# Kernel tuning notes

Hardware: AMD Instinct MI355X
Metric: run time of the kernel (lower is better)

The kernel has to match this reference:

```python
import jax, jax.numpy as jnp
import numpy as np

B, S, D_MODEL, H = 4, 4096, 1024, 16
HD = D_MODEL // H  # 64
KS = 3             # depthwise conv kernel size
EPS = 1e-6


def dw_causal_conv(x, w, b):
    """Causal depthwise conv over seq. x: [B,S,H,Dk], w: [Dk,KS], b: [Dk].
    Matches Conv1d(groups=d_k, padding=KS-1) followed by cropping the last KS-1."""
    s = x.shape[1]
    xp = jnp.pad(x, ((0, 0), (KS - 1, 0), (0, 0), (0, 0)))
    y = b  # broadcast over [B,S,H,Dk]
    for j in range(KS):
        y = y + w[:, j] * xp[:, j:j + s]
    return y


def feature_map(x):
    return jax.nn.elu(x) + 1.0


def setup_inputs() -> dict:
    key = jax.random.key(0)
    ks = jax.random.split(key, 20)
    sc = 0.02
    inp = {
        'query': jax.random.normal(ks[0], (B, S, D_MODEL), jnp.float32),
        'key':   jax.random.normal(ks[1], (B, S, D_MODEL), jnp.float32),
        'value': jax.random.normal(ks[2], (B, S, D_MODEL), jnp.float32),
        'q_w': jax.random.normal(ks[3], (D_MODEL, D_MODEL), jnp.float32) * sc,
        'q_b': jax.random.normal(ks[4], (D_MODEL,), jnp.float32) * sc,
        'k_w': jax.random.normal(ks[5], (D_MODEL, D_MODEL), jnp.float32) * sc,
        'k_b': jax.random.normal(ks[6], (D_MODEL,), jnp.float32) * sc,
        'v_w': jax.random.normal(ks[7], (D_MODEL, D_MODEL), jnp.float32) * sc,
        'v_b': jax.random.normal(ks[8], (D_MODEL,), jnp.float32) * sc,
        'o_w': jax.random.normal(ks[9], (D_MODEL, D_MODEL), jnp.float32) * sc,
        'o_b': jax.random.normal(ks[10], (D_MODEL,), jnp.float32) * sc,
        'qc_w': jax.random.normal(ks[11], (HD, KS), jnp.float32) * 0.3,
        'qc_b': jax.random.normal(ks[12], (HD,), jnp.float32) * 0.02,
        'kc_w': jax.random.normal(ks[13], (HD, KS), jnp.float32) * 0.3,
        'kc_b': jax.random.normal(ks[14], (HD,), jnp.float32) * 0.02,
        'vc_w': jax.random.normal(ks[15], (HD, KS), jnp.float32) * 0.3,
        'vc_b': jax.random.normal(ks[16], (HD,), jnp.float32) * 0.02,
    }
    return inp


def reference(query, key, value, q_w, q_b, k_w, k_b, v_w, v_b, o_w, o_b,
              qc_w, qc_b, kc_w, kc_b, vc_w, vc_b):
    b, s, _ = query.shape
    q = (query @ q_w.T + q_b).reshape(b, s, H, HD)
    k = (key   @ k_w.T + k_b).reshape(b, s, H, HD)
    v = (value @ v_w.T + v_b).reshape(b, s, H, HD)

    q = feature_map(dw_causal_conv(q, qc_w, qc_b))
    k = feature_map(dw_causal_conv(k, kc_w, kc_b))
    v = dw_causal_conv(v, vc_w, vc_b)

    # linear attention: [B,S,H,D] -> [B,H,S,D]
    Q = q.transpose(0, 2, 1, 3)
    K = k.transpose(0, 2, 1, 3)
    V = v.transpose(0, 2, 1, 3)
    KV = jnp.einsum('bhsd,bhse->bhde', K, V)            # [B,H,D,D]
    Z = 1.0 / jnp.einsum('bhsd,bhd->bhs', Q, K.sum(axis=2) + EPS)
    V_new = jnp.einsum('bhde,bhsd,bhs->bhse', KV, Q, Z)  # [B,H,S,D]

    out = V_new.transpose(0, 2, 1, 3).reshape(b, s, D_MODEL)
    return out @ o_w.T + o_b
```

## Files before the change

### kernel.cpp

```cpp
#include <hip/hip_runtime.h>
#include <hip/hip_bf16.h>
#include <math.h>

#define BB 4
#define SS 4096
#define DM 1024
#define HH 16
#define HD 64
#define NTOK (BB * SS)
#define TSZ ((size_t)NTOK * DM)

typedef _Float16 half8 __attribute__((ext_vector_type(8)));
typedef _Float16 half4v __attribute__((ext_vector_type(4)));
typedef float floatx4 __attribute__((ext_vector_type(4)));

__device__ __forceinline__ void gload16(const void* g, void* l) {
  __builtin_amdgcn_global_load_lds(
      (const __attribute__((address_space(1))) void*)g,
      (__attribute__((address_space(3))) void*)l, 16, 0, 0);
}

#define WAIT4 asm volatile("s_waitcnt vmcnt(4)" ::: "memory")
#define WAIT2 asm volatile("s_waitcnt vmcnt(2)" ::: "memory")
#define WAIT0 asm volatile("s_waitcnt vmcnt(0)" ::: "memory")
#define BARR __builtin_amdgcn_s_barrier()

#define MM3(A_, ah_, al_, bh_, bl_)                                   \
  A_ = __builtin_amdgcn_mfma_f32_16x16x32_f16(ah_, bh_, A_, 0, 0, 0); \
  A_ = __builtin_amdgcn_mfma_f32_16x16x32_f16(ah_, bl_, A_, 0, 0, 0); \
  A_ = __builtin_amdgcn_mfma_f32_16x16x32_f16(al_, bh_, A_, 0, 0, 0)

__device__ __forceinline__ void cvhl(const float4 u0, const float4 u1,
                                     half8& h, half8& l) {
  const float a[8] = {u0.x, u0.y, u0.z, u0.w, u1.x, u1.y, u1.z, u1.w};
#pragma unroll
  for (int e = 0; e < 8; ++e) {
    const _Float16 hh = (_Float16)a[e];
    h[e] = hh;
    l[e] = (_Float16)(a[e] - (float)hh);
  }
}

__global__ __launch_bounds__(256) void split_w4(
    const float* __restrict__ w0, const float* __restrict__ w1,
    const float* __restrict__ w2, const float* __restrict__ w3,
    _Float16* __restrict__ hi, _Float16* __restrict__ lo) {
  const int wi = blockIdx.y;
  const float* src = (wi == 0) ? w0 : (wi == 1) ? w1 : (wi == 2) ? w2 : w3;
  const int i = blockIdx.x * 256 + threadIdx.x;
  const size_t off = ((size_t)wi << 20) >> 2;
  const float4 x = ((const float4*)src)[i];
  half4v h, l;
  h.x = (_Float16)x.x; l.x = (_Float16)(x.x - (float)h.x);
  h.y = (_Float16)x.y; l.y = (_Float16)(x.y - (float)h.y);
  h.z = (_Float16)x.z; l.z = (_Float16)(x.z - (float)h.z);
  h.w = (_Float16)x.w; l.w = (_Float16)(x.w - (float)h.w);
  ((half4v*)hi)[off + i] = h;
  ((half4v*)lo)[off + i] = l;
}

__global__ __launch_bounds__(512, 2) void qkv_gemm8(
    const float* __restrict__ Ak, const float* __restrict__ Av,
    const float* __restrict__ Aq, const _Float16* __restrict__ WhiA,
    const _Float16* __restrict__ WloA, const float* __restrict__ bk,
    const float* __restrict__ bv, const float* __restrict__ bq,
    float* __restrict__ Ck, float* __restrict__ Cv, float* __restrict__ Cq) {
  __shared__ float sA[2][256 * 32];
  __shared__ _Float16 sB[2][256 * 64];

  const int z = blockIdx.z;
  const float* A = (z == 0) ? Ak : (z == 1) ? Av : Aq;
  const float* bias = (z == 0) ? bk : (z == 1) ? bv : bq;
  float* C = (z == 0) ? Ck : (z == 1) ? Cv : Cq;
  const _Float16* Whi = WhiA + ((size_t)z << 20);
  const _Float16* Wlo = WloA + ((size_t)z << 20);

  const int t = threadIdx.x;
  const int wav = t >> 6, lane = t & 63;
  const int wr = wav >> 2, wc = wav & 3;

  const int wg = blockIdx.y * 4 + blockIdx.x;
  const int xcd = wg & 7, cidx = wg >> 3;
  const int bm = ((xcd >> 1) * 16 + (cidx >> 1)) * 256;
  const int bn = ((xcd & 1) * 2 + (cidx & 1)) * 256;

  const int lrow = wav * 8 + (lane >> 3);
  const int cpr = (lane & 7) ^ (lane >> 3);
  const float* pA0 = A + (size_t)(bm + lrow) * DM + cpr * 4;
  const _Float16* pB0 =
      ((cpr < 4) ? Whi : Wlo) + (size_t)(bn + lrow) * DM + (cpr & 3) * 8;
  const int ldsArow = wav * 8 * 32;
  const int ldsBrow = wav * 8 * 64;

#define STA(buf, rb, k0) \
  gload16(pA0 + (size_t)(rb) * DM + (k0), &sA[buf][(rb) * 32 + ldsArow])
#define STB(buf, rb, k0) \
  gload16(pB0 + (size_t)(rb) * DM + (k0), &sB[buf][(rb) * 64 + ldsBrow])

  STA(0, 0, 0); STA(0, 64, 0);
  STB(0, 0, 0); STB(0, 64, 0);
  STB(0, 128, 0); STB(0, 192, 0);
  STA(0, 128, 0); STA(0, 192, 0);

  const int fm = lane & 15;
  const int sw = fm & 7;
  const int kq = lane >> 4;
  int baseA[4], baseB[2];
#pragma unroll
  for (int i = 0; i < 4; ++i) baseA[i] = (wr * 64 + i * 16 + fm) * 32;
#pragma unroll
  for (int j = 0; j < 2; ++j) baseB[j] = (wc * 32 + j * 16 + fm) * 64;
  const int aS0 = ((kq * 2) ^ sw) * 4;
  const int aS1 = ((kq * 2 + 1) ^ sw) * 4;
  const int bSh = (kq ^ sw) * 8;
  const int bSl = ((kq + 4) ^ sw) * 8;

  floatx4 acc[2][4][2][2];
#pragma unroll
  for (int qm = 0; qm < 2; ++qm)
#pragma unroll
    for (int i = 0; i < 4; ++i)
#pragma unroll
      for (int qn = 0; qn < 2; ++qn)
#pragma unroll
        for (int j = 0; j < 2; ++j)
          acc[qm][i][qn][j] = (floatx4){0.f, 0.f, 0.f, 0.f};

  half8 ah[4], al[4];

#define READA_Q(cur_, QM)                                       \
  _Pragma("unroll") for (int i_ = 0; i_ < 4; ++i_) {            \
    const float4 u0_ =                                          \
        *(const float4*)&sA[cur_][baseA[i_] + (QM) * 4096 + aS0]; \
    const float4 u1_ =                                          \
        *(const float4*)&sA[cur_][baseA[i_] + (QM) * 4096 + aS1]; \
    cvhl(u0_, u1_, ah[i_], al[i_]);                             \
  }

#define PH_Q(cur_, QM, QN, ...)                                   \
  {                                                               \
    const half8 bh0_ =                                            \
        *(const half8*)&sB[cur_][baseB[0] + (QN) * 8192 + bSh];   \
    const half8 bl0_ =                                            \
        *(const half8*)&sB[cur_][baseB[0] + (QN) * 8192 + bSl];   \
    const half8 bh1_ =                                            \
        *(const half8*)&sB[cur_][baseB[1] + (QN) * 8192 + bSh];   \
    const half8 bl1_ =                                            \
        *(const half8*)&sB[cur_][baseB[1] + (QN) * 8192 + bSl];   \
    __VA_ARGS__;                                                  \
    __builtin_amdgcn_s_setprio(1);                                \
    _Pragma("unroll") for (int i_ = 0; i_ < 4; ++i_) {            \
      MM3(acc[QM][i_][QN][0], ah[i_], al[i_], bh0_, bl0_);        \
      MM3(acc[QM][i_][QN][1], ah[i_], al[i_], bh1_, bl1_);        \
    }                                                             \
    __builtin_amdgcn_s_setprio(0);                                \
  }

  for (int tt = 0; tt < 31; ++tt) {
    const int cur = tt & 1, nxt = cur ^ 1;
    const int k1 = tt * 32 + 32;
    WAIT4; BARR;
    READA_Q(cur, 0);
    PH_Q(cur, 0, 0, STA(nxt, 0, k1); STA(nxt, 64, k1));
    WAIT4; BARR;
    PH_Q(cur, 0, 1, STB(nxt, 0, k1); STB(nxt, 64, k1));
    WAIT4; BARR;
    READA_Q(cur, 1);
    PH_Q(cur, 1, 0, STB(nxt, 128, k1); STB(nxt, 192, k1));
    PH_Q(cur, 1, 1, STA(nxt, 128, k1); STA(nxt, 192, k1));
  }
  WAIT4; BARR;
  READA_Q(1, 0);
  PH_Q(1, 0, 0, (void)0);
  WAIT2; BARR;
  PH_Q(1, 0, 1, (void)0);
  WAIT0; BARR;
  READA_Q(1, 1);
  PH_Q(1, 1, 0, (void)0);
  PH_Q(1, 1, 1, (void)0);

  const int cr = kq * 4;
#pragma unroll
  for (int qm = 0; qm < 2; ++qm)
#pragma unroll
    for (int i = 0; i < 4; ++i) {
      const int grow = bm + qm * 128 + wr * 64 + i * 16 + cr;
#pragma unroll
      for (int qn = 0; qn < 2; ++qn)
#pragma unroll
        for (int j = 0; j < 2; ++j) {
          const int gcol = bn + qn * 128 + wc * 32 + j * 16 + fm;
          const float bo = bias[gcol];
#pragma unroll
          for (int r = 0; r < 4; ++r)
            C[(size_t)(grow + r) * DM + gcol] = acc[qm][i][qn][j][r] + bo;
        }
    }
#undef STA
#undef STB
#undef READA_Q
#undef PH_Q
}

__global__ __launch_bounds__(512, 2) void o_gemm8(
    const _Float16* __restrict__ Ahi, const _Float16* __restrict__ Alo,
    const _Float16* __restrict__ Whi, const _Float16* __restrict__ Wlo,
    const float* __restrict__ bias, float* __restrict__ C) {
  __shared__ _Float16 sA[2][256 * 64];
  __shared__ _Float16 sB[2][256 * 64];

  const int t = threadIdx.x;
  const int wav = t >> 6, lane = t & 63;
  const int wr = wav >> 2, wc = wav & 3;

  const int wg = blockIdx.y * 4 + blockIdx.x;
  const int xcd = wg & 7, cidx = wg >> 3;
  const int bm = ((xcd >> 1) * 16 + (cidx >> 1)) * 256;
  const int bn = ((xcd & 1) * 2 + (cidx & 1)) * 256;

  const int lrow = wav * 8 + (lane >> 3);
  const int cpr = (lane & 7) ^ (lane >> 3);
  const _Float16* pA0 =
      ((cpr < 4) ? Ahi : Alo) + (size_t)(bm + lrow) * DM + (cpr & 3) * 8;
  const _Float16* pB0 =
      ((cpr < 4) ? Whi : Wlo) + (size_t)(bn + lrow) * DM + (cpr & 3) * 8;
  const int ldsRow = wav * 8 * 64;

#define STAO(buf, rb, k0) \
  gload16(pA0 + (size_t)(rb) * DM + (k0), &sA[buf][(rb) * 64 + ldsRow])
#define STBO(buf, rb, k0) \
  gload16(pB0 + (size_t)(rb) * DM + (k0), &sB[buf][(rb) * 64 + ldsRow])

  STAO(0, 0, 0); STAO(0, 64, 0);
  STBO(0, 0, 0); STBO(0, 64, 0);
  STBO(0, 128, 0); STBO(0, 192, 0);
  STAO(0, 128, 0); STAO(0, 192, 0);

  const int fm = lane & 15;
  const int sw = fm & 7;
  const int kq = lane >> 4;
  int baseA[4], baseB[2];
#pragma unroll
  for (int i = 0; i < 4; ++i) baseA[i] = (wr * 64 + i * 16 + fm) * 64;
#pragma unroll
  for (int j = 0; j < 2; ++j) baseB[j] = (wc * 32 + j * 16 + fm) * 64;
  const int bSh = (kq ^ sw) * 8;
  const int bSl = ((kq + 4) ^ sw) * 8;

  floatx4 acc[2][4][2][2];
#pragma unroll
  for (int qm = 0; qm < 2; ++qm)
#pragma unroll
    for (int i = 0; i < 4; ++i)
#pragma unroll
      for (int qn = 0; qn < 2; ++qn)
#pragma unroll
        for (int j = 0; j < 2; ++j)
          acc[qm][i][qn][j] = (floatx4){0.f, 0.f, 0.f, 0.f};

  half8 ah[4], al[4];

#define READA_O(cur_, QM)                                                 \
  _Pragma("unroll") for (int i_ = 0; i_ < 4; ++i_) {                      \
    ah[i_] = *(const half8*)&sA[cur_][baseA[i_] + (QM) * 8192 + bSh];     \
    al[i_] = *(const half8*)&sA[cur_][baseA[i_] + (QM) * 8192 + bSl];     \
  }

#define PH_O(cur_, QM, QN, ...)                                   \
  {                                                               \
    const half8 bh0_ =                                            \
        *(const half8*)&sB[cur_][baseB[0] + (QN) * 8192 + bSh];   \
    const half8 bl0_ =                                            \
        *(const half8*)&sB[cur_][baseB[0] + (QN) * 8192 + bSl];   \
    const half8 bh1_ =                                            \
        *(const half8*)&sB[cur_][baseB[1] + (QN) * 8192 + bSh];   \
    const half8 bl1_ =                                            \
        *(const half8*)&sB[cur_][baseB[1] + (QN) * 8192 + bSl];   \
    __VA_ARGS__;                                                  \
    __builtin_amdgcn_s_setprio(1);                                \
    _Pragma("unroll") for (int i_ = 0; i_ < 4; ++i_) {            \
      MM3(acc[QM][i_][QN][0], ah[i_], al[i_], bh0_, bl0_);        \
      MM3(acc[QM][i_][QN][1], ah[i_], al[i_], bh1_, bl1_);        \
    }                                                             \
    __builtin_amdgcn_s_setprio(0);                                \
  }

  for (int tt = 0; tt < 31; ++tt) {
    const int cur = tt & 1, nxt = cur ^ 1;
    const int k1 = tt * 32 + 32;
    WAIT4; BARR;
    READA_O(cur, 0);
    PH_O(cur, 0, 0, STAO(nxt, 0, k1); STAO(nxt, 64, k1));
    WAIT4; BARR;
    PH_O(cur, 0, 1, STBO(nxt, 0, k1); STBO(nxt, 64, k1));
    WAIT4; BARR;
    READA_O(cur, 1);
    PH_O(cur, 1, 0, STBO(nxt, 128, k1); STBO(nxt, 192, k1));
    PH_O(cur, 1, 1, STAO(nxt, 128, k1); STAO(nxt, 192, k1));
  }
  WAIT4; BARR;
  READA_O(1, 0);
  PH_O(1, 0, 0, (void)0);
  WAIT2; BARR;
  PH_O(1, 0, 1, (void)0);
  WAIT0; BARR;
  READA_O(1, 1);
  PH_O(1, 1, 0, (void)0);
  PH_O(1, 1, 1, (void)0);

  const int cr = kq * 4;
#pragma unroll
  for (int qm = 0; qm < 2; ++qm)
#pragma unroll
    for (int i = 0; i < 4; ++i) {
      const int grow = bm + qm * 128 + wr * 64 + i * 16 + cr;
#pragma unroll
      for (int qn = 0; qn < 2; ++qn)
#pragma unroll
        for (int j = 0; j < 2; ++j) {
          const int gcol = bn + qn * 128 + wc * 32 + j * 16 + fm;
          const float bo = bias[gcol];
#pragma unroll
          for (int r = 0; r < 4; ++r)
            C[(size_t)(grow + r) * DM + gcol] = acc[qm][i][qn][j][r] + bo;
        }
    }
#undef STAO
#undef STBO
#undef READA_O
#undef PH_O
}

__global__ __launch_bounds__(256) void kv_accum_conv(
    const float* __restrict__ Kg, const float* __restrict__ Vg,
    const float* __restrict__ kc_w, const float* __restrict__ kc_b,
    const float* __restrict__ vc_w, const float* __restrict__ vc_b,
    float* __restrict__ KVp, float* __restrict__ Ksp) {
  const int bh = blockIdx.x;
  const int b = bh >> 4, h = bh & 15;
  const int chunk = blockIdx.y;
  const int s0 = chunk * 256;
  const int t = threadIdx.x;
  const int w = t >> 6, lane = t & 63;
  __shared__ float Kr[34][64], Vr[34][64];
  __shared__ float Kc[32][64], Vc[32][64];
  __shared__ float kw0[64], kw1[64], kw2[64], kb_[64];
  __shared__ float vw0[64], vw1[64], vw2[64], vb_[64];

  if (t < 64) {
    kw0[t] = kc_w[t * 3 + 0]; kw1[t] = kc_w[t * 3 + 1]; kw2[t] = kc_w[t * 3 + 2];
    vw0[t] = vc_w[t * 3 + 0]; vw1[t] = vc_w[t * 3 + 1]; vw2[t] = vc_w[t * 3 + 2];
    kb_[t] = kc_b[t]; vb_[t] = vc_b[t];
  }

  const int d0 = w * 16 + (lane >> 4) * 4;
  const int e0 = (lane & 15) * 4;
  float acc[4][4];
#pragma unroll
  for (int i = 0; i < 4; ++i)
#pragma unroll
    for (int j = 0; j < 4; ++j) acc[i][j] = 0.f;
  float4 ks = make_float4(0.f, 0.f, 0.f, 0.f);
  const size_t gbase = (size_t)b * SS * DM + h * HD;

  for (int c = 0; c < 256; c += 32) {
    __syncthreads();
    for (int idx = t; idx < 544; idx += 256) {
      const int row = idx >> 4, col = (idx & 15) * 4;
      const int s = s0 + c - 2 + row;
      float4 k4 = make_float4(0.f, 0.f, 0.f, 0.f);
      float4 v4 = make_float4(0.f, 0.f, 0.f, 0.f);
      if (s >= 0) {
        k4 = *(const float4*)&Kg[gbase + (size_t)s * DM + col];
        v4 = *(const float4*)&Vg[gbase + (size_t)s * DM + col];
      }
      *(float4*)&Kr[row][col] = k4;
      *(float4*)&Vr[row][col] = v4;
    }
    __syncthreads();
    for (int idx = t; idx < 2048; idx += 256) {
      const int row = idx >> 6, dd = idx & 63;
      float yk = kb_[dd] + kw0[dd] * Kr[row][dd] + kw1[dd] * Kr[row + 1][dd] +
                 kw2[dd] * Kr[row + 2][dd];
      Kc[row][dd] = (yk > 0.f) ? (yk + 1.f) : expf(yk);
      Vc[row][dd] = vb_[dd] + vw0[dd] * Vr[row][dd] + vw1[dd] * Vr[row + 1][dd] +
                    vw2[dd] * Vr[row + 2][dd];
    }
    __syncthreads();
#pragma unroll 2
    for (int ss = 0; ss < 32; ++ss) {
      const float4 k4 = *(const float4*)&Kc[ss][d0];
      const float4 v4 = *(const float4*)&Vc[ss][e0];
      ks.x += k4.x; ks.y += k4.y; ks.z += k4.z; ks.w += k4.w;
      const float kk[4] = {k4.x, k4.y, k4.z, k4.w};
      const float vv[4] = {v4.x, v4.y, v4.z, v4.w};
#pragma unroll
      for (int i = 0; i < 4; ++i)
#pragma unroll
        for (int j = 0; j < 4; ++j) acc[i][j] = fmaf(kk[i], vv[j], acc[i][j]);
    }
  }
  float* kvp = &KVp[((size_t)(bh * 16 + chunk)) * 4096];
#pragma unroll
  for (int i = 0; i < 4; ++i) {
    float4 o = make_float4(acc[i][0], acc[i][1], acc[i][2], acc[i][3]);
    *(float4*)&kvp[(d0 + i) * 64 + e0] = o;
  }
  if ((lane & 15) == 0) {
    float* kp = &Ksp[(bh * 16 + chunk) * 64 + d0];
    kp[0] = ks.x; kp[1] = ks.y; kp[2] = ks.z; kp[3] = ks.w;
  }
}

__global__ __launch_bounds__(256) void kv_reduce(
    const float* __restrict__ KVp, const float* __restrict__ Ksp,
    float* __restrict__ KV, float* __restrict__ Ksum) {
  const int bh = blockIdx.x;
  const int t = threadIdx.x;
  for (int i = t; i < 4096; i += 256) {
    float s = 0.f;
#pragma unroll
    for (int c = 0; c < 16; ++c) s += KVp[((size_t)(bh * 16 + c)) * 4096 + i];
    KV[(size_t)bh * 4096 + i] = s;
  }
  if (t < 64) {
    float s = 1e-6f;
#pragma unroll
    for (int c = 0; c < 16; ++c) s += Ksp[(bh * 16 + c) * 64 + t];
    Ksum[bh * 64 + t] = s;
  }
}

__global__ __launch_bounds__(256) void attn_apply_conv(
    const float* __restrict__ Qg, const float* __restrict__ KV,
    const float* __restrict__ Ksum, const float* __restrict__ qc_w,
    const float* __restrict__ qc_b, _Float16* __restrict__ OHi,
    _Float16* __restrict__ OLo) {
  const int bh = blockIdx.x;
  const int b = bh >> 4, h = bh & 15;
  const int s0 = blockIdx.y * 64;
  const int t = threadIdx.x;
  const int w = t >> 6, lane = t & 63;
  __shared__ float Qr[66][64];
  __shared__ float QsT[64][68];
// ... 95 lines not shown
  const float* k_b = (const float*)d_in[6];
  const float* v_w = (const float*)d_in[7];
  const float* v_b = (const float*)d_in[8];
  const float* o_w = (const float*)d_in[9];
  const float* o_b = (const float*)d_in[10];
  const float* qc_w = (const float*)d_in[11];
  const float* qc_b = (const float*)d_in[12];
  const float* kc_w = (const float*)d_in[13];
  const float* kc_b = (const float*)d_in[14];
  const float* vc_w = (const float*)d_in[15];
  const float* vc_b = (const float*)d_in[16];
  float* out = (float*)d_out;

  float* ws = (float*)d_ws;
  float* buf0 = ws;
  float* buf1 = ws + TSZ;
  float* buf2 = ws + 2 * TSZ;
  _Float16* Whi = (_Float16*)(ws + 3 * TSZ);
  _Float16* Wlo = Whi + 4 * (1 << 20);
  float* KVp  = (float*)(Wlo + 4 * (1 << 20));
  float* Ksp  = KVp + (size_t)64 * 16 * 4096;
  float* KV   = Ksp + 64 * 16 * 64;
  float* Ksum = KV + (size_t)64 * 4096;

  _Float16* WhiO = Whi + 3 * (1 << 20);
  _Float16* WloO = Wlo + 3 * (1 << 20);
  _Float16* OHi = (_Float16*)buf0;
  _Float16* OLo = OHi + TSZ;

  const int nW4 = DM * DM / 4;

  split_w4<<<dim3(nW4 / 256, 4), 256, 0, stream>>>(k_w, v_w, q_w, o_w, Whi, Wlo);

  qkv_gemm8<<<dim3(4, 64, 3), 512, 0, stream>>>(
      key, value, query, Whi, Wlo, k_b, v_b, q_b, buf0, buf1, buf2);

  kv_accum_conv<<<dim3(64, 16), 256, 0, stream>>>(buf0, buf1, kc_w, kc_b, vc_w,
                                                  vc_b, KVp, Ksp);
  kv_reduce<<<64, 256, 0, stream>>>(KVp, Ksp, KV, Ksum);

  attn_apply_conv<<<dim3(64, 64), 256, 0, stream>>>(buf2, KV, Ksum, qc_w, qc_b,
                                                    OHi, OLo);

  o_gemm8<<<dim3(4, 64), 512, 0, stream>>>(OHi, OLo, WhiO, WloO, o_b, out);
}
```

Before: 705.5 us.

## Use 32x32 MFMA in GEMMs, merge QKV into one persistent pass, prefetch conv loads

```diff
diff --git a/kernel.cpp b/kernel.cpp
--- a/kernel.cpp
+++ b/kernel.cpp
@@ -13,6 +13,7 @@
 typedef _Float16 half8 __attribute__((ext_vector_type(8)));
 typedef _Float16 half4v __attribute__((ext_vector_type(4)));
 typedef float floatx4 __attribute__((ext_vector_type(4)));
+typedef float floatx16 __attribute__((ext_vector_type(16)));
 
 __device__ __forceinline__ void gload16(const void* g, void* l) {
   __builtin_amdgcn_global_load_lds(
@@ -25,10 +26,10 @@
 #define WAIT0 asm volatile("s_waitcnt vmcnt(0)" ::: "memory")
 #define BARR __builtin_amdgcn_s_barrier()
 
-#define MM3(A_, ah_, al_, bh_, bl_)                                   \
-  A_ = __builtin_amdgcn_mfma_f32_16x16x32_f16(ah_, bh_, A_, 0, 0, 0); \
-  A_ = __builtin_amdgcn_mfma_f32_16x16x32_f16(ah_, bl_, A_, 0, 0, 0); \
-  A_ = __builtin_amdgcn_mfma_f32_16x16x32_f16(al_, bh_, A_, 0, 0, 0)
+#define MM3W(A_, ah_, al_, bh_, bl_)                                   \
+  A_ = __builtin_amdgcn_mfma_f32_32x32x16_f16(ah_, bh_, A_, 0, 0, 0);  \
+  A_ = __builtin_amdgcn_mfma_f32_32x32x16_f16(ah_, bl_, A_, 0, 0, 0);  \
+  A_ = __builtin_amdgcn_mfma_f32_32x32x16_f16(al_, bh_, A_, 0, 0, 0)
 
 __device__ __forceinline__ void cvhl(const float4 u0, const float4 u1,
                                      half8& h, half8& l) {
@@ -59,7 +60,7 @@
   ((half4v*)lo)[off + i] = l;
 }
 
-__global__ __launch_bounds__(512, 2) void qkv_gemm8(
+__global__ __launch_bounds__(512, 2) void qkv_gemm32(
     const float* __restrict__ Ak, const float* __restrict__ Av,
     const float* __restrict__ Aq, const _Float16* __restrict__ WhiA,
     const _Float16* __restrict__ WloA, const float* __restrict__ bk,
@@ -68,13 +69,6 @@
   __shared__ float sA[2][256 * 32];
   __shared__ _Float16 sB[2][256 * 64];
 
-  const int z = blockIdx.z;
-  const float* A = (z == 0) ? Ak : (z == 1) ? Av : Aq;
-  const float* bias = (z == 0) ? bk : (z == 1) ? bv : bq;
-  float* C = (z == 0) ? Ck : (z == 1) ? Cv : Cq;
-  const _Float16* Whi = WhiA + ((size_t)z << 20);
-  const _Float16* Wlo = WloA + ((size_t)z << 20);
-
   const int t = threadIdx.x;
   const int wav = t >> 6, lane = t & 63;
   const int wr = wav >> 2, wc = wav & 3;
@@ -86,123 +80,135 @@
 
   const int lrow = wav * 8 + (lane >> 3);
   const int cpr = (lane & 7) ^ (lane >> 3);
-  const float* pA0 = A + (size_t)(bm + lrow) * DM + cpr * 4;
-  const _Float16* pB0 =
-      ((cpr < 4) ? Whi : Wlo) + (size_t)(bn + lrow) * DM + (cpr & 3) * 8;
+  const float* pA0k = Ak + (size_t)(bm + lrow) * DM + cpr * 4;
+  const float* pA0v = Av + (size_t)(bm + lrow) * DM + cpr * 4;
+  const float* pA0q = Aq + (size_t)(bm + lrow) * DM + cpr * 4;
+  const _Float16* pB0z =
+      ((cpr < 4) ? WhiA : WloA) + (size_t)(bn + lrow) * DM + (cpr & 3) * 8;
   const int ldsArow = wav * 8 * 32;
   const int ldsBrow = wav * 8 * 64;
 
-#define STA(buf, rb, k0) \
-  gload16(pA0 + (size_t)(rb) * DM + (k0), &sA[buf][(rb) * 32 + ldsArow])
-#define STB(buf, rb, k0) \
-  gload16(pB0 + (size_t)(rb) * DM + (k0), &sB[buf][(rb) * 64 + ldsBrow])
-
-  STA(0, 0, 0); STA(0, 64, 0);
-  STB(0, 0, 0); STB(0, 64, 0);
-  STB(0, 128, 0); STB(0, 192, 0);
-  STA(0, 128, 0); STA(0, 192, 0);
-
-  const int fm = lane & 15;
-  const int sw = fm & 7;
-  const int kq = lane >> 4;
-  int baseA[4], baseB[2];
-#pragma unroll
-  for (int i = 0; i < 4; ++i) baseA[i] = (wr * 64 + i * 16 + fm) * 32;
-#pragma unroll
-  for (int j = 0; j < 2; ++j) baseB[j] = (wc * 32 + j * 16 + fm) * 64;
-  const int aS0 = ((kq * 2) ^ sw) * 4;
-  const int aS1 = ((kq * 2 + 1) ^ sw) * 4;
-  const int bSh = (kq ^ sw) * 8;
-  const int bSl = ((kq + 4) ^ sw) * 8;
-
-  floatx4 acc[2][4][2][2];
-#pragma unroll
-  for (int qm = 0; qm < 2; ++qm)
-#pragma unroll
-    for (int i = 0; i < 4; ++i)
-#pragma unroll
-      for (int qn = 0; qn < 2; ++qn)
+#define STA(ap, buf, rb, kk) \
+  gload16((ap) + (size_t)(rb) * DM + (kk), &sA[buf][(rb) * 32 + ldsArow])
+#define STB(bp, buf, rb, kk) \
+  gload16((bp) + (size_t)(rb) * DM + (kk), &sB[buf][(rb) * 64 + ldsBrow])
+
+  STA(pA0k, 0, 0, 0); STA(pA0k, 0, 64, 0);
+  STB(pB0z, 0, 0, 0); STB(pB0z, 0, 64, 0);
+  STB(pB0z, 0, 128, 0); STB(pB0z, 0, 192, 0);
+  STA(pA0k, 0, 128, 0); STA(pA0k, 0, 192, 0);
+
+  const int sw8 = lane & 7;
+  const int kg = lane >> 5;
+  const int sh0 = ((kg) ^ sw8) * 8,     slo0 = ((kg + 4) ^ sw8) * 8;
+  const int sh1 = ((2 + kg) ^ sw8) * 8, slo1 = ((2 + kg + 4) ^ sw8) * 8;
+  const int a00 = ((2 * kg) ^ sw8) * 4,     a01 = ((2 * kg + 1) ^ sw8) * 4;
+  const int a10 = ((4 + 2 * kg) ^ sw8) * 4, a11 = ((5 + 2 * kg) ^ sw8) * 4;
+
+  floatx16 acc[2][2][2];
+  floatx16 zz;
+#pragma unroll
+  for (int e = 0; e < 16; ++e) zz[e] = 0.f;
+#pragma unroll
+  for (int i = 0; i < 2; ++i)
+#pragma unroll
+    for (int j = 0; j < 2; ++j)
+#pragma unroll
+      for (int k = 0; k < 2; ++k) acc[i][j][k] = zz;
+
+  half8 ah[2][2], al[2][2];
+
+#define READA32(cur_, QM)                                                  \
+  _Pragma("unroll") for (int mt_ = 0; mt_ < 2; ++mt_) {                    \
+    const int ar_ = ((QM) * 128 + wr * 64 + mt_ * 32 + (lane & 31)) * 32;  \
+    const float4 u0_ = *(const float4*)&sA[cur_][ar_ + a00];               \
+    const float4 u1_ = *(const float4*)&sA[cur_][ar_ + a01];               \
+    cvhl(u0_, u1_, ah[mt_][0], al[mt_][0]);                                \
+    const float4 u2_ = *(const float4*)&sA[cur_][ar_ + a10];               \
+    const float4 u3_ = *(const float4*)&sA[cur_][ar_ + a11];               \
+    cvhl(u2_, u3_, ah[mt_][1], al[mt_][1]);                                \
+  }
+
+#define PH32(cur_, QM, QN, ...)                                            \
+  {                                                                        \
+    const int br_ = ((QN) * 128 + wc * 32 + (lane & 31)) * 64;             \
+    const half8 bh0_ = *(const half8*)&sB[cur_][br_ + sh0];                \
+    const half8 bl0_ = *(const half8*)&sB[cur_][br_ + slo0];               \
+    const half8 bh1_ = *(const half8*)&sB[cur_][br_ + sh1];                \
+    const half8 bl1_ = *(const half8*)&sB[cur_][br_ + slo1];               \
+    __VA_ARGS__;                                                           \
+    __builtin_amdgcn_s_setprio(1);                                         \
+    MM3W(acc[QM][0][QN], ah[0][0], al[0][0], bh0_, bl0_);                  \
+    MM3W(acc[QM][1][QN], ah[1][0], al[1][0], bh0_, bl0_);                  \
+    MM3W(acc[QM][0][QN], ah[0][1], al[0][1], bh1_, bl1_);                  \
+    MM3W(acc[QM][1][QN], ah[1][1], al[1][1], bh1_, bl1_);                  \
+    __builtin_amdgcn_s_setprio(0);                                         \
+  }
+
+#define CWRITE(Cp_, bp_)                                                   \
+  {                                                                        \
+    _Pragma("unroll") for (int qn_ = 0; qn_ < 2; ++qn_) {                  \
+      const int gcol = bn + qn_ * 128 + wc * 32 + (lane & 31);             \
+      const float bo = (bp_)[gcol];                                        \
+      _Pragma("unroll") for (int qm_ = 0; qm_ < 2; ++qm_)                  \
+      _Pragma("unroll") for (int mt_ = 0; mt_ < 2; ++mt_) {                \
+        const int rbase = bm + qm_ * 128 + wr * 64 + mt_ * 32 + 4 * kg;    \
+        _Pragma("unroll") for (int r_ = 0; r_ < 16; ++r_) {                \
+          const int grow = rbase + (r_ & 3) + 8 * (r_ >> 2);               \
+          (Cp_)[(size_t)grow * DM + gcol] = acc[qm_][mt_][qn_][r_] + bo;   \
+        }                                                                  \
+      }                                                                    \
+    }                                                                      \
+  }
+
+  for (int tt = 0; tt < 95; ++tt) {
+    const int cur = tt & 1, nxt = cur ^ 1;
+    const int tn = tt + 1;
+    const int zn = tn >> 5;
+    const int kn = (tn & 31) * 32;
+    const float* aN = (zn == 0) ? pA0k : (zn == 1) ? pA0v : pA0q;
+    const _Float16* bN = pB0z + ((size_t)zn << 20);
+    WAIT4; BARR;
+    READA32(cur, 0);
+    PH32(cur, 0, 0, STA(aN, nxt, 0, kn); STA(aN, nxt, 64, kn));
+    WAIT4; BARR;
+    PH32(cur, 0, 1, STB(bN, nxt, 0, kn); STB(bN, nxt, 64, kn));
+    WAIT4; BARR;
+    READA32(cur, 1);
+    PH32(cur, 1, 0, STB(bN, nxt, 128, kn); STB(bN, nxt, 192, kn));
+    PH32(cur, 1, 1, STA(aN, nxt, 128, kn); STA(aN, nxt, 192, kn));
+    if ((tt & 31) == 31) {
+      const int zc = tt >> 5;
+      float* Cp = (zc == 0) ? Ck : Cv;
+      const float* bp = (zc == 0) ? bk : bv;
+      CWRITE(Cp, bp);
+      WAIT0;
+#pragma unroll
+      for (int i = 0; i < 2; ++i)
 #pragma unroll
         for (int j = 0; j < 2; ++j)
-          acc[qm][i][qn][j] = (floatx4){0.f, 0.f, 0.f, 0.f};
-
-  half8 ah[4], al[4];
-
-#define READA_Q(cur_, QM)                                       \
-  _Pragma("unroll") for (int i_ = 0; i_ < 4; ++i_) {            \
-    const float4 u0_ =                                          \
-        *(const float4*)&sA[cur_][baseA[i_] + (QM) * 4096 + aS0]; \
-    const float4 u1_ =                                          \
-        *(const float4*)&sA[cur_][baseA[i_] + (QM) * 4096 + aS1]; \
-    cvhl(u0_, u1_, ah[i_], al[i_]);                             \
-  }
-
-#define PH_Q(cur_, QM, QN, ...)                                   \
-  {                                                               \
-    const half8 bh0_ =                                            \
-        *(const half8*)&sB[cur_][baseB[0] + (QN) * 8192 + bSh];   \
-    const half8 bl0_ =                                            \
-        *(const half8*)&sB[cur_][baseB[0] + (QN) * 8192 + bSl];   \
-    const half8 bh1_ =                                            \
-        *(const half8*)&sB[cur_][baseB[1] + (QN) * 8192 + bSh];   \
-    const half8 bl1_ =                                            \
-        *(const half8*)&sB[cur_][baseB[1] + (QN) * 8192 + bSl];   \
-    __VA_ARGS__;                                                  \
-    __builtin_amdgcn_s_setprio(1);                                \
-    _Pragma("unroll") for (int i_ = 0; i_ < 4; ++i_) {            \
-      MM3(acc[QM][i_][QN][0], ah[i_], al[i_], bh0_, bl0_);        \
-      MM3(acc[QM][i_][QN][1], ah[i_], al[i_], bh1_, bl1_);        \
-    }                                                             \
-    __builtin_amdgcn_s_setprio(0);                                \
-  }
-
-  for (int tt = 0; tt < 31; ++tt) {
-    const int cur = tt & 1, nxt = cur ^ 1;
-    const int k1 = tt * 32 + 32;
-    WAIT4; BARR;
-    READA_Q(cur, 0);
-    PH_Q(cur, 0, 0, STA(nxt, 0, k1); STA(nxt, 64, k1));
-    WAIT4; BARR;
-    PH_Q(cur, 0, 1, STB(nxt, 0, k1); STB(nxt, 64, k1));
-    WAIT4; BARR;
-    READA_Q(cur, 1);
-    PH_Q(cur, 1, 0, STB(nxt, 128, k1); STB(nxt, 192, k1));
-    PH_Q(cur, 1, 1, STA(nxt, 128, k1); STA(nxt, 192, k1));
+#pragma unroll
+          for (int k = 0; k < 2; ++k) acc[i][j][k] = zz;
+    }
   }
   WAIT4; BARR;
-  READA_Q(1, 0);
-  PH_Q(1, 0, 0, (void)0);
+  READA32(1, 0);
+  PH32(1, 0, 0, (void)0);
   WAIT2; BARR;
-  PH_Q(1, 0, 1, (void)0);
+  PH32(1, 0, 1, (void)0);
   WAIT0; BARR;
-  READA_Q(1, 1);
-  PH_Q(1, 1, 0, (void)0);
-  PH_Q(1, 1, 1, (void)0);
-
-  const int cr = kq * 4;
-#pragma unroll
-  for (int qm = 0; qm < 2; ++qm)
-#pragma unroll
-    for (int i = 0; i < 4; ++i) {
-      const int grow = bm + qm * 128 + wr * 64 + i * 16 + cr;
-#pragma unroll
-      for (int qn = 0; qn < 2; ++qn)
-#pragma unroll
-        for (int j = 0; j < 2; ++j) {
-          const int gcol = bn + qn * 128 + wc * 32 + j * 16 + fm;
-          const float bo = bias[gcol];
-#pragma unroll
-          for (int r = 0; r < 4; ++r)
-            C[(size_t)(grow + r) * DM + gcol] = acc[qm][i][qn][j][r] + bo;
-        }
-    }
+  READA32(1, 1);
+  PH32(1, 1, 0, (void)0);
+  PH32(1, 1, 1, (void)0);
+  CWRITE(Cq, bq);
 #undef STA
 #undef STB
-#undef READA_Q
-#undef PH_Q
-}
-
-__global__ __launch_bounds__(512, 2) void o_gemm8(
+#undef READA32
+#undef PH32
+#undef CWRITE
+}
+
+__global__ __launch_bounds__(512, 2) void o_gemm32(
     const _Float16* __restrict__ Ahi, const _Float16* __restrict__ Alo,
     const _Float16* __restrict__ Whi, const _Float16* __restrict__ Wlo,
     const float* __restrict__ bias, float* __restrict__ C) {
@@ -226,109 +232,102 @@
       ((cpr < 4) ? Whi : Wlo) + (size_t)(bn + lrow) * DM + (cpr & 3) * 8;
   const int ldsRow = wav * 8 * 64;
 
-#define STAO(buf, rb, k0) \
-  gload16(pA0 + (size_t)(rb) * DM + (k0), &sA[buf][(rb) * 64 + ldsRow])
-#define STBO(buf, rb, k0) \
-  gload16(pB0 + (size_t)(rb) * DM + (k0), &sB[buf][(rb) * 64 + ldsRow])
+#define STAO(buf, rb, kk) \
+  gload16(pA0 + (size_t)(rb) * DM + (kk), &sA[buf][(rb) * 64 + ldsRow])
+#define STBO(buf, rb, kk) \
+  gload16(pB0 + (size_t)(rb) * DM + (kk), &sB[buf][(rb) * 64 + ldsRow])
 
   STAO(0, 0, 0); STAO(0, 64, 0);
   STBO(0, 0, 0); STBO(0, 64, 0);
   STBO(0, 128, 0); STBO(0, 192, 0);
   STAO(0, 128, 0); STAO(0, 192, 0);
 
-  const int fm = lane & 15;
-  const int sw = fm & 7;
-  const int kq = lane >> 4;
-  int baseA[4], baseB[2];
-#pragma unroll
-  for (int i = 0; i < 4; ++i) baseA[i] = (wr * 64 + i * 16 + fm) * 64;
-#pragma unroll
-  for (int j = 0; j < 2; ++j) baseB[j] = (wc * 32 + j * 16 + fm) * 64;
-  const int bSh = (kq ^ sw) * 8;
-  const int bSl = ((kq + 4) ^ sw) * 8;
-
-  floatx4 acc[2][4][2][2];
-#pragma unroll
-  for (int qm = 0; qm < 2; ++qm)
-#pragma unroll
-    for (int i = 0; i < 4; ++i)
-#pragma unroll
-      for (int qn = 0; qn < 2; ++qn)
-#pragma unroll
-        for (int j = 0; j < 2; ++j)
-          acc[qm][i][qn][j] = (floatx4){0.f, 0.f, 0.f, 0.f};
-
-  half8 ah[4], al[4];
-
-#define READA_O(cur_, QM)                                                 \
-  _Pragma("unroll") for (int i_ = 0; i_ < 4; ++i_) {                      \
-    ah[i_] = *(const half8*)&sA[cur_][baseA[i_] + (QM) * 8192 + bSh];     \
-    al[i_] = *(const half8*)&sA[cur_][baseA[i_] + (QM) * 8192 + bSl];     \
-  }
-
-#define PH_O(cur_, QM, QN, ...)                                   \
-  {                                                               \
-    const half8 bh0_ =                                            \
-        *(const half8*)&sB[cur_][baseB[0] + (QN) * 8192 + bSh];   \
-    const half8 bl0_ =                                            \
-        *(const half8*)&sB[cur_][baseB[0] + (QN) * 8192 + bSl];   \
-    const half8 bh1_ =                                            \
-        *(const half8*)&sB[cur_][baseB[1] + (QN) * 8192 + bSh];   \
-    const half8 bl1_ =                                            \
-        *(const half8*)&sB[cur_][baseB[1] + (QN) * 8192 + bSl];   \
-    __VA_ARGS__;                                                  \
-    __builtin_amdgcn_s_setprio(1);                                \
-    _Pragma("unroll") for (int i_ = 0; i_ < 4; ++i_) {            \
-      MM3(acc[QM][i_][QN][0], ah[i_], al[i_], bh0_, bl0_);        \
-      MM3(acc[QM][i_][QN][1], ah[i_], al[i_], bh1_, bl1_);        \
-    }                                                             \
-    __builtin_amdgcn_s_setprio(0);                                \
+  const int sw8 = lane & 7;
+  const int kg = lane >> 5;
+  const int sh0 = ((kg) ^ sw8) * 8,     slo0 = ((kg + 4) ^ sw8) * 8;
+  const int sh1 = ((2 + kg) ^ sw8) * 8, slo1 = ((2 + kg + 4) ^ sw8) * 8;
+
+  floatx16 acc[2][2][2];
+  floatx16 zz;
+#pragma unroll
+  for (int e = 0; e < 16; ++e) zz[e] = 0.f;
+#pragma unroll
+  for (int i = 0; i < 2; ++i)
+#pragma unroll
+    for (int j = 0; j < 2; ++j)
+#pragma unroll
+      for (int k = 0; k < 2; ++k) acc[i][j][k] = zz;
+
+  half8 ah[2][2], al[2][2];
+
+#define READAO(cur_, QM)                                                   \
+  _Pragma("unroll") for (int mt_ = 0; mt_ < 2; ++mt_) {                    \
+    const int ar_ = ((QM) * 128 + wr * 64 + mt_ * 32 + (lane & 31)) * 64;  \
+    ah[mt_][0] = *(const half8*)&sA[cur_][ar_ + sh0];                      \
+    al[mt_][0] = *(const half8*)&sA[cur_][ar_ + slo0];                     \
+    ah[mt_][1] = *(const half8*)&sA[cur_][ar_ + sh1];                      \
+    al[mt_][1] = *(const half8*)&sA[cur_][ar_ + slo1];                     \
+  }
+
+#define PHO(cur_, QM, QN, ...)                                             \
+  {                                                                        \
+    const int br_ = ((QN) * 128 + wc * 32 + (lane & 31)) * 64;             \
+    const half8 bh0_ = *(const half8*)&sB[cur_][br_ + sh0];                \
+    const half8 bl0_ = *(const half8*)&sB[cur_][br_ + slo0];               \
+    const half8 bh1_ = *(const half8*)&sB[cur_][br_ + sh1];                \
+    const half8 bl1_ = *(const half8*)&sB[cur_][br_ + slo1];               \
+    __VA_ARGS__;                                                           \
+    __builtin_amdgcn_s_setprio(1);                                         \
+    MM3W(acc[QM][0][QN], ah[0][0], al[0][0], bh0_, bl0_);                  \
+    MM3W(acc[QM][1][QN], ah[1][0], al[1][0], bh0_, bl0_);                  \
+    MM3W(acc[QM][0][QN], ah[0][1], al[0][1], bh1_, bl1_);                  \
+    MM3W(acc[QM][1][QN], ah[1][1], al[1][1], bh1_, bl1_);                  \
+    __builtin_amdgcn_s_setprio(0);                                         \
   }
 
   for (int tt = 0; tt < 31; ++tt) {
     const int cur = tt & 1, nxt = cur ^ 1;
     const int k1 = tt * 32 + 32;
     WAIT4; BARR;
-    READA_O(cur, 0);
-    PH_O(cur, 0, 0, STAO(nxt, 0, k1); STAO(nxt, 64, k1));
+    READAO(cur, 0);
+    PHO(cur, 0, 0, STAO(nxt, 0, k1); STAO(nxt, 64, k1));
     WAIT4; BARR;
-    PH_O(cur, 0, 1, STBO(nxt, 0, k1); STBO(nxt, 64, k1));
+    PHO(cur, 0, 1, STBO(nxt, 0, k1); STBO(nxt, 64, k1));
     WAIT4; BARR;
-    READA_O(cur, 1);
-    PH_O(cur, 1, 0, STBO(nxt, 128, k1); STBO(nxt, 192, k1));
-    PH_O(cur, 1, 1, STAO(nxt, 128, k1); STAO(nxt, 192, k1));
+    READAO(cur, 1);
+    PHO(cur, 1, 0, STBO(nxt, 128, k1); STBO(nxt, 192, k1));
+    PHO(cur, 1, 1, STAO(nxt, 128, k1); STAO(nxt, 192, k1));
   }
   WAIT4; BARR;
-  READA_O(1, 0);
-  PH_O(1, 0, 0, (void)0);
+  READAO(1, 0);
+  PHO(1, 0, 0, (void)0);
   WAIT2; BARR;
-  PH_O(1, 0, 1, (void)0);
+  PHO(1, 0, 1, (void)0);
   WAIT0; BARR;
-  READA_O(1, 1);
-  PH_O(1, 1, 0, (void)0);
-  PH_O(1, 1, 1, (void)0);
-
-  const int cr = kq * 4;
-#pragma unroll
-  for (int qm = 0; qm < 2; ++qm)
-#pragma unroll
-    for (int i = 0; i < 4; ++i) {
-      const int grow = bm + qm * 128 + wr * 64 + i * 16 + cr;
-#pragma unroll
-      for (int qn = 0; qn < 2; ++qn)
-#pragma unroll
-        for (int j = 0; j < 2; ++j) {
-          const int gcol = bn + qn * 128 + wc * 32 + j * 16 + fm;
-          const float bo = bias[gcol];
-#pragma unroll
-          for (int r = 0; r < 4; ++r)
-            C[(size_t)(grow + r) * DM + gcol] = acc[qm][i][qn][j][r] + bo;
+  READAO(1, 1);
+  PHO(1, 1, 0, (void)0);
+  PHO(1, 1, 1, (void)0);
+
+#pragma unroll
+  for (int qn_ = 0; qn_ < 2; ++qn_) {
+    const int gcol = bn + qn_ * 128 + wc * 32 + (lane & 31);
+    const float bo = bias[gcol];
+#pragma unroll
+    for (int qm_ = 0; qm_ < 2; ++qm_)
+#pragma unroll
+      for (int mt_ = 0; mt_ < 2; ++mt_) {
+        const int rbase = bm + qm_ * 128 + wr * 64 + mt_ * 32 + 4 * kg;
+#pragma unroll
+        for (int r_ = 0; r_ < 16; ++r_) {
+          const int grow = rbase + (r_ & 3) + 8 * (r_ >> 2);
+          C[(size_t)grow * DM + gcol] = acc[qm_][mt_][qn_][r_] + bo;
         }
-    }
+      }
+  }
 #undef STAO
 #undef STBO
-#undef READA_O
-#undef PH_O
+#undef READAO
+#undef PHO
 }
 
 __global__ __launch_bounds__(256) void kv_accum_conv(
@@ -363,20 +362,36 @@
   float4 ks = make_float4(0.f, 0.f, 0.f, 0.f);
   const size_t gbase = (size_t)b * SS * DM + h * HD;
 
+  float4 kpre[3], vpre[3];
+#define KVFETCH(cc)                                                        \
+  _Pragma("unroll") for (int u = 0; u < 3; ++u) {                          \
+    const int idx = t + u * 256;                                           \
+    if (idx < 544) {                                                       \
+      const int row = idx >> 4, col = (idx & 15) * 4;                      \
+      const int s = s0 + (cc) - 2 + row;                                   \
+      float4 k4 = make_float4(0.f, 0.f, 0.f, 0.f);                         \
+      float4 v4 = make_float4(0.f, 0.f, 0.f, 0.f);                         \
+      if (s >= 0) {                                                        \
+        k4 = *(const float4*)&Kg[gbase + (size_t)s * DM + col];            \
+        v4 = *(const float4*)&Vg[gbase + (size_t)s * DM + col];            \
+      }                                                                    \
+      kpre[u] = k4; vpre[u] = v4;                                          \
+    }                                                                      \
+  }
+#define KVWRITE                                                            \
+  _Pragma("unroll") for (int u = 0; u < 3; ++u) {                          \
+    const int idx = t + u * 256;                                           \
+    if (idx < 544) {                                                       \
+      const int row = idx >> 4, col = (idx & 15) * 4;                      \
+      *(float4*)&Kr[row][col] = kpre[u];                                   \
+      *(float4*)&Vr[row][col] = vpre[u];                                   \
+    }                                                                      \
+  }
+
+  KVFETCH(0);
   for (int c = 0; c < 256; c += 32) {
     __syncthreads();
-    for (int idx = t; idx < 544; idx += 256) {
-      const int row = idx >> 4, col = (idx & 15) * 4;
-      const int s = s0 + c - 2 + row;
-      float4 k4 = make_float4(0.f, 0.f, 0.f, 0.f);
-      float4 v4 = make_float4(0.f, 0.f, 0.f, 0.f);
-      if (s >= 0) {
-        k4 = *(const float4*)&Kg[gbase + (size_t)s * DM + col];
-        v4 = *(const float4*)&Vg[gbase + (size_t)s * DM + col];
-      }
-      *(float4*)&Kr[row][col] = k4;
-      *(float4*)&Vr[row][col] = v4;
-    }
+    KVWRITE;
     __syncthreads();
     for (int idx = t; idx < 2048; idx += 256) {
       const int row = idx >> 6, dd = idx & 63;
@@ -386,6 +401,7 @@
       Vc[row][dd] = vb_[dd] + vw0[dd] * Vr[row][dd] + vw1[dd] * Vr[row + 1][dd] +
                     vw2[dd] * Vr[row + 2][dd];
     }
+    if (c + 32 < 256) KVFETCH(c + 32);
     __syncthreads();
 #pragma unroll 2
     for (int ss = 0; ss < 32; ++ss) {
@@ -410,6 +426,8 @@
     float* kp = &Ksp[(bh * 16 + chunk) * 64 + d0];
     kp[0] = ks.x; kp[1] = ks.y; kp[2] = ks.z; kp[3] = ks.w;
   }
+#undef KVFETCH
+#undef KVWRITE
 }
 
 __global__ __launch_bounds__(256) void kv_reduce(
@@ -571,7 +589,7 @@
 
   split_w4<<<dim3(nW4 / 256, 4), 256, 0, stream>>>(k_w, v_w, q_w, o_w, Whi, Wlo);
 
-  qkv_gemm8<<<dim3(4, 64, 3), 512, 0, stream>>>(
+  qkv_gemm32<<<dim3(4, 64), 512, 0, stream>>>(
       key, value, query, Whi, Wlo, k_b, v_b, q_b, buf0, buf1, buf2);
 
   kv_accum_conv<<<dim3(64, 16), 256, 0, stream>>>(buf0, buf1, kc_w, kc_b, vc_w,
@@ -581,5 +599,5 @@
   attn_apply_conv<<<dim3(64, 64), 256, 0, stream>>>(buf2, KV, Ksum, qc_w, qc_b,
                                                     OHi, OLo);
 
-  o_gemm8<<<dim3(4, 64), 512, 0, stream>>>(OHi, OLo, WhiO, WloO, o_b, out);
-}
+  o_gemm32<<<dim3(4, 64), 512, 0, stream>>>(OHi, OLo, WhiO, WloO, o_b, out);
+}
```

Measured after the change: 785.0 us. 11.3% more time.

## Reuse B fragments across M halves in GEMMs and prefetch KV tiles into registers

Applied to the files above, without the earlier changes.

```diff
diff --git a/kernel.cpp b/kernel.cpp
--- a/kernel.cpp
+++ b/kernel.cpp
@@ -117,16 +117,18 @@
 
   floatx4 acc[2][4][2][2];
 #pragma unroll
-  for (int qm = 0; qm < 2; ++qm)
-#pragma unroll
-    for (int i = 0; i < 4; ++i)
-#pragma unroll
-      for (int qn = 0; qn < 2; ++qn)
-#pragma unroll
-        for (int j = 0; j < 2; ++j)
-          acc[qm][i][qn][j] = (floatx4){0.f, 0.f, 0.f, 0.f};
+  for (int i = 0; i < 2; ++i)
+#pragma unroll
+    for (int j = 0; j < 4; ++j)
+#pragma unroll
+      for (int k = 0; k < 2; ++k)
+#pragma unroll
+        for (int l = 0; l < 2; ++l)
+          acc[i][j][k][l] = (floatx4){0.f, 0.f, 0.f, 0.f};
 
   half8 ah[4], al[4];
+  half8 b0h0, b0l0, b0h1, b0l1;
+  half8 b1h0, b1l0, b1h1, b1l1;
 
 #define READA_Q(cur_, QM)                                       \
   _Pragma("unroll") for (int i_ = 0; i_ < 4; ++i_) {            \
@@ -137,49 +139,57 @@
     cvhl(u0_, u1_, ah[i_], al[i_]);                             \
   }
 
-#define PH_Q(cur_, QM, QN, ...)                                   \
-  {                                                               \
-    const half8 bh0_ =                                            \
-        *(const half8*)&sB[cur_][baseB[0] + (QN) * 8192 + bSh];   \
-    const half8 bl0_ =                                            \
-        *(const half8*)&sB[cur_][baseB[0] + (QN) * 8192 + bSl];   \
-    const half8 bh1_ =                                            \
-        *(const half8*)&sB[cur_][baseB[1] + (QN) * 8192 + bSh];   \
-    const half8 bl1_ =                                            \
-        *(const half8*)&sB[cur_][baseB[1] + (QN) * 8192 + bSl];   \
-    __VA_ARGS__;                                                  \
-    __builtin_amdgcn_s_setprio(1);                                \
-    _Pragma("unroll") for (int i_ = 0; i_ < 4; ++i_) {            \
-      MM3(acc[QM][i_][QN][0], ah[i_], al[i_], bh0_, bl0_);        \
-      MM3(acc[QM][i_][QN][1], ah[i_], al[i_], bh1_, bl1_);        \
-    }                                                             \
-    __builtin_amdgcn_s_setprio(0);                                \
-  }
+#define RB_Q(cur_, QN, H0, L0, H1, L1)                          \
+  H0 = *(const half8*)&sB[cur_][baseB[0] + (QN) * 8192 + bSh];  \
+  L0 = *(const half8*)&sB[cur_][baseB[0] + (QN) * 8192 + bSl];  \
+  H1 = *(const half8*)&sB[cur_][baseB[1] + (QN) * 8192 + bSh];  \
+  L1 = *(const half8*)&sB[cur_][baseB[1] + (QN) * 8192 + bSl]
+
+#define MFMACL(QM, QN, H0, L0, H1, L1)                          \
+  __builtin_amdgcn_s_setprio(1);                                \
+  _Pragma("unroll") for (int i_ = 0; i_ < 4; ++i_) {            \
+    MM3(acc[QM][i_][QN][0], ah[i_], al[i_], H0, L0);            \
+    MM3(acc[QM][i_][QN][1], ah[i_], al[i_], H1, L1);            \
+  }                                                             \
+  __builtin_amdgcn_s_setprio(0)
 
   for (int tt = 0; tt < 31; ++tt) {
     const int cur = tt & 1, nxt = cur ^ 1;
     const int k1 = tt * 32 + 32;
     WAIT4; BARR;
     READA_Q(cur, 0);
-    PH_Q(cur, 0, 0, STA(nxt, 0, k1); STA(nxt, 64, k1));
+    RB_Q(cur, 0, b0h0, b0l0, b0h1, b0l1);
+    STA(nxt, 0, k1); STA(nxt, 64, k1);
+    MFMACL(0, 0, b0h0, b0l0, b0h1, b0l1);
+    BARR;
     WAIT4; BARR;
-    PH_Q(cur, 0, 1, STB(nxt, 0, k1); STB(nxt, 64, k1));
+    RB_Q(cur, 1, b1h0, b1l0, b1h1, b1l1);
+    STB(nxt, 0, k1); STB(nxt, 64, k1);
+    MFMACL(0, 1, b1h0, b1l0, b1h1, b1l1);
+    BARR;
     WAIT4; BARR;
     READA_Q(cur, 1);
-    PH_Q(cur, 1, 0, STB(nxt, 128, k1); STB(nxt, 192, k1));
-    PH_Q(cur, 1, 1, STA(nxt, 128, k1); STA(nxt, 192, k1));
+    STB(nxt, 128, k1); STB(nxt, 192, k1);
+    MFMACL(1, 0, b0h0, b0l0, b0h1, b0l1);
+    BARR;
+    STA(nxt, 128, k1); STA(nxt, 192, k1);
+    MFMACL(1, 1, b1h0, b1l0, b1h1, b1l1);
   }
   WAIT4; BARR;
   READA_Q(1, 0);
-  PH_Q(1, 0, 0, (void)0);
+  RB_Q(1, 0, b0h0, b0l0, b0h1, b0l1);
+  MFMACL(0, 0, b0h0, b0l0, b0h1, b0l1);
+  BARR;
   WAIT2; BARR;
-  PH_Q(1, 0, 1, (void)0);
+  RB_Q(1, 1, b1h0, b1l0, b1h1, b1l1);
+  MFMACL(0, 1, b1h0, b1l0, b1h1, b1l1);
+  BARR;
   WAIT0; BARR;
   READA_Q(1, 1);
-  PH_Q(1, 1, 0, (void)0);
-  PH_Q(1, 1, 1, (void)0);
-
-  const int cr = kq * 4;
+  MFMACL(1, 0, b0h0, b0l0, b0h1, b0l1);
+  MFMACL(1, 1, b1h0, b1l0, b1h1, b1l1);
+
+  const int cr = (lane >> 4) * 4;
 #pragma unroll
   for (int qm = 0; qm < 2; ++qm)
 #pragma unroll
@@ -199,7 +209,8 @@
 #undef STA
 #undef STB
 #undef READA_Q
-#undef PH_Q
+#undef RB_Q
+#undef MFMACL
 }
 
 __global__ __launch_bounds__(512, 2) void o_gemm8(
@@ -249,16 +260,18 @@
 
   floatx4 acc[2][4][2][2];
 #pragma unroll
-  for (int qm = 0; qm < 2; ++qm)
-#pragma unroll
-    for (int i = 0; i < 4; ++i)
-#pragma unroll
-      for (int qn = 0; qn < 2; ++qn)
-#pragma unroll
-        for (int j = 0; j < 2; ++j)
-          acc[qm][i][qn][j] = (floatx4){0.f, 0.f, 0.f, 0.f};
+  for (int i = 0; i < 2; ++i)
+#pragma unroll
+    for (int j = 0; j < 4; ++j)
+#pragma unroll
+      for (int k = 0; k < 2; ++k)
+#pragma unroll
+        for (int l = 0; l < 2; ++l)
+          acc[i][j][k][l] = (floatx4){0.f, 0.f, 0.f, 0.f};
 
   half8 ah[4], al[4];
+  half8 b0h0, b0l0, b0h1, b0l1;
+  half8 b1h0, b1l0, b1h1, b1l1;
 
 #define READA_O(cur_, QM)                                                 \
   _Pragma("unroll") for (int i_ = 0; i_ < 4; ++i_) {                      \
@@ -266,49 +279,57 @@
     al[i_] = *(const half8*)&sA[cur_][baseA[i_] + (QM) * 8192 + bSl];     \
   }
 
-#define PH_O(cur_, QM, QN, ...)                                   \
-  {                                                               \
-    const half8 bh0_ =                                            \
-        *(const half8*)&sB[cur_][baseB[0] + (QN) * 8192 + bSh];   \
-    const half8 bl0_ =                                            \
-        *(const half8*)&sB[cur_][baseB[0] + (QN) * 8192 + bSl];   \
-    const half8 bh1_ =                                            \
-        *(const half8*)&sB[cur_][baseB[1] + (QN) * 8192 + bSh];   \
-    const half8 bl1_ =                                            \
-        *(const half8*)&sB[cur_][baseB[1] + (QN) * 8192 + bSl];   \
-    __VA_ARGS__;                                                  \
-    __builtin_amdgcn_s_setprio(1);                                \
-    _Pragma("unroll") for (int i_ = 0; i_ < 4; ++i_) {            \
-      MM3(acc[QM][i_][QN][0], ah[i_], al[i_], bh0_, bl0_);        \
-      MM3(acc[QM][i_][QN][1], ah[i_], al[i_], bh1_, bl1_);        \
-    }                                                             \
-    __builtin_amdgcn_s_setprio(0);                                \
-  }
+#define RB_O(cur_, QN, H0, L0, H1, L1)                          \
+  H0 = *(const half8*)&sB[cur_][baseB[0] + (QN) * 8192 + bSh];  \
+  L0 = *(const half8*)&sB[cur_][baseB[0] + (QN) * 8192 + bSl];  \
+  H1 = *(const half8*)&sB[cur_][baseB[1] + (QN) * 8192 + bSh];  \
+  L1 = *(const half8*)&sB[cur_][baseB[1] + (QN) * 8192 + bSl]
+
+#define MFMACLO(QM, QN, H0, L0, H1, L1)                         \
+  __builtin_amdgcn_s_setprio(1);                                \
+  _Pragma("unroll") for (int i_ = 0; i_ < 4; ++i_) {            \
+    MM3(acc[QM][i_][QN][0], ah[i_], al[i_], H0, L0);            \
+    MM3(acc[QM][i_][QN][1], ah[i_], al[i_], H1, L1);            \
+  }                                                             \
+  __builtin_amdgcn_s_setprio(0)
 
   for (int tt = 0; tt < 31; ++tt) {
     const int cur = tt & 1, nxt = cur ^ 1;
     const int k1 = tt * 32 + 32;
     WAIT4; BARR;
     READA_O(cur, 0);
-    PH_O(cur, 0, 0, STAO(nxt, 0, k1); STAO(nxt, 64, k1));
+    RB_O(cur, 0, b0h0, b0l0, b0h1, b0l1);
+    STAO(nxt, 0, k1); STAO(nxt, 64, k1);
+    MFMACLO(0, 0, b0h0, b0l0, b0h1, b0l1);
+    BARR;
     WAIT4; BARR;
-    PH_O(cur, 0, 1, STBO(nxt, 0, k1); STBO(nxt, 64, k1));
+    RB_O(cur, 1, b1h0, b1l0, b1h1, b1l1);
+    STBO(nxt, 0, k1); STBO(nxt, 64, k1);
+    MFMACLO(0, 1, b1h0, b1l0, b1h1, b1l1);
+    BARR;
     WAIT4; BARR;
     READA_O(cur, 1);
-    PH_O(cur, 1, 0, STBO(nxt, 128, k1); STBO(nxt, 192, k1));
-    PH_O(cur, 1, 1, STAO(nxt, 128, k1); STAO(nxt, 192, k1));
+    STBO(nxt, 128, k1); STBO(nxt, 192, k1);
+    MFMACLO(1, 0, b0h0, b0l0, b0h1, b0l1);
+    BARR;
+    STAO(nxt, 128, k1); STAO(nxt, 192, k1);
+    MFMACLO(1, 1, b1h0, b1l0, b1h1, b1l1);
   }
   WAIT4; BARR;
   READA_O(1, 0);
-  PH_O(1, 0, 0, (void)0);
+  RB_O(1, 0, b0h0, b0l0, b0h1, b0l1);
+  MFMACLO(0, 0, b0h0, b0l0, b0h1, b0l1);
+  BARR;
   WAIT2; BARR;
-  PH_O(1, 0, 1, (void)0);
+  RB_O(1, 1, b1h0, b1l0, b1h1, b1l1);
+  MFMACLO(0, 1, b1h0, b1l0, b1h1, b1l1);
+  BARR;
   WAIT0; BARR;
   READA_O(1, 1);
-  PH_O(1, 1, 0, (void)0);
-  PH_O(1, 1, 1, (void)0);
-
-  const int cr = kq * 4;
+  MFMACLO(1, 0, b0h0, b0l0, b0h1, b0l1);
+  MFMACLO(1, 1, b1h0, b1l0, b1h1, b1l1);
+
+  const int cr = (lane >> 4) * 4;
 #pragma unroll
   for (int qm = 0; qm < 2; ++qm)
 #pragma unroll
@@ -328,7 +349,8 @@
 #undef STAO
 #undef STBO
 #undef READA_O
-#undef PH_O
+#undef RB_O
+#undef MFMACLO
 }
 
 __global__ __launch_bounds__(256) void kv_accum_conv(
@@ -363,20 +385,36 @@
   float4 ks = make_float4(0.f, 0.f, 0.f, 0.f);
   const size_t gbase = (size_t)b * SS * DM + h * HD;
 
+  float4 kpre[3], vpre[3];
+#define KVFETCH(cc)                                                        \
+  _Pragma("unroll") for (int u = 0; u < 3; ++u) {                          \
+    const int idx = t + u * 256;                                           \
+    if (idx < 544) {                                                       \
+      const int row = idx >> 4, col = (idx & 15) * 4;                      \
+      const int s = s0 + (cc) - 2 + row;                                   \
+      float4 k4 = make_float4(0.f, 0.f, 0.f, 0.f);                         \
+      float4 v4 = make_float4(0.f, 0.f, 0.f, 0.f);                         \
+      if (s >= 0) {                                                        \
+        k4 = *(const float4*)&Kg[gbase + (size_t)s * DM + col];            \
+        v4 = *(const float4*)&Vg[gbase + (size_t)s * DM + col];            \
+      }                                                                    \
+      kpre[u] = k4; vpre[u] = v4;                                          \
+    }                                                                      \
+  }
+#define KVWRITE                                                            \
+  _Pragma("unroll") for (int u = 0; u < 3; ++u) {                          \
+    const int idx = t + u * 256;                                           \
+    if (idx < 544) {                                                       \
+      const int row = idx >> 4, col = (idx & 15) * 4;                      \
+      *(float4*)&Kr[row][col] = kpre[u];                                   \
+      *(float4*)&Vr[row][col] = vpre[u];                                   \
+    }                                                                      \
+  }
+
+  KVFETCH(0);
   for (int c = 0; c < 256; c += 32) {
     __syncthreads();
-    for (int idx = t; idx < 544; idx += 256) {
-      const int row = idx >> 4, col = (idx & 15) * 4;
-      const int s = s0 + c - 2 + row;
-      float4 k4 = make_float4(0.f, 0.f, 0.f, 0.f);
-      float4 v4 = make_float4(0.f, 0.f, 0.f, 0.f);
-      if (s >= 0) {
-        k4 = *(const float4*)&Kg[gbase + (size_t)s * DM + col];
-        v4 = *(const float4*)&Vg[gbase + (size_t)s * DM + col];
-      }
-      *(float4*)&Kr[row][col] = k4;
-      *(float4*)&Vr[row][col] = v4;
-    }
+    KVWRITE;
     __syncthreads();
     for (int idx = t; idx < 2048; idx += 256) {
       const int row = idx >> 6, dd = idx & 63;
@@ -386,6 +424,7 @@
       Vc[row][dd] = vb_[dd] + vw0[dd] * Vr[row][dd] + vw1[dd] * Vr[row + 1][dd] +
                     vw2[dd] * Vr[row + 2][dd];
     }
+    if (c + 32 < 256) KVFETCH(c + 32);
     __syncthreads();
 #pragma unroll 2
     for (int ss = 0; ss < 32; ++ss) {
@@ -410,6 +449,8 @@
     float* kp = &Ksp[(bh * 16 + chunk) * 64 + d0];
     kp[0] = ks.x; kp[1] = ks.y; kp[2] = ks.z; kp[3] = ks.w;
   }
+#undef KVFETCH
+#undef KVWRITE
 }
 
 __global__ __launch_bounds__(256) void kv_reduce(
```

After: 722.5 us. 1.02x slower.
